# Performance work log

Hardware: AMD Instinct MI355X
Metric: run time of the kernel (lower is better)

## Reference

```python
import jax, jax.numpy as jnp
import numpy as np

ENC_DIM, PRED_DIM, JOINT_DIM, VOCAB = 512, 640, 512, 1024

def setup_inputs() -> dict:
    key = jax.random.key(0)
    ks = jax.random.split(key, 8)
    s = lambda d: 1.0 / np.sqrt(d)
    return {
        "enc_out": jax.random.normal(ks[0], (8, 256, ENC_DIM), jnp.float32),
        "pred_out": jax.random.normal(ks[1], (8, 64, PRED_DIM), jnp.float32),
        "W_enc": jax.random.uniform(ks[2], (ENC_DIM, JOINT_DIM), jnp.float32, -s(ENC_DIM), s(ENC_DIM)),
        "b_enc": jax.random.uniform(ks[3], (JOINT_DIM,), jnp.float32, -s(ENC_DIM), s(ENC_DIM)),
        "W_pred": jax.random.uniform(ks[4], (PRED_DIM, JOINT_DIM), jnp.float32, -s(PRED_DIM), s(PRED_DIM)),
        "b_pred": jax.random.uniform(ks[5], (JOINT_DIM,), jnp.float32, -s(PRED_DIM), s(PRED_DIM)),
        "W_joint": jax.random.uniform(ks[6], (JOINT_DIM, VOCAB), jnp.float32, -s(JOINT_DIM), s(JOINT_DIM)),
        "b_joint": jax.random.uniform(ks[7], (VOCAB,), jnp.float32, -s(JOINT_DIM), s(JOINT_DIM)),
    }

def reference(enc_out, pred_out, W_enc, b_enc, W_pred, b_pred, W_joint, b_joint):
    # (B,T,J) and (B,U,J) projections
    enc_p = jnp.einsum('btd,dj->btj', enc_out, W_enc) + b_enc
    pred_p = jnp.einsum('bud,dj->buj', pred_out, W_pred) + b_pred
    # broadcast add -> (B,T,U,J), tanh, project to vocab
    joint = jnp.tanh(enc_p[:, :, None, :] + pred_p[:, None, :, :])
    logits = jnp.einsum('btuj,jv->btuv', joint, W_joint) + b_joint
    return logits
```

## Files before the change

### kernel.cpp

```cpp
#include <hip/hip_runtime.h>
#include <hip/hip_bf16.h>
#include <stdint.h>

#define B_    8
#define T_    256
#define U_    64
#define JD    512
#define VD    1024
#define ROWS  (B_*T_*U_)
#define MTOT  (B_*T_)
#define UROWS (B_*U_)

typedef __attribute__((ext_vector_type(8))) short short8;
typedef __attribute__((ext_vector_type(4))) float f32x4;

__device__ __forceinline__ unsigned short f2bf(float f) {
  unsigned u = __float_as_uint(f);
  u += 0x7fffu + ((u >> 16) & 1u);
  return (unsigned short)(u >> 16);
}
__device__ __forceinline__ float fast_tanh(float x) {
  float e = __builtin_amdgcn_exp2f(x * 2.8853900817779268f);
  return 1.0f - 2.0f * __builtin_amdgcn_rcpf(e + 1.0f);
}

__device__ __forceinline__ void pack_w_body(const float* __restrict__ W,
                                            unsigned short* __restrict__ dst,
                                            int K, int N, int t) {
  int lane = t & 63;
  int rest = t >> 6;
  int kch  = K >> 5;
  int kc   = rest % kch;
  int nt   = rest / kch;
  int krow = (kc << 5) + ((lane >> 4) << 3);
  int col  = (nt << 4) + (lane & 15);
  unsigned short v[8];
#pragma unroll
  for (int j = 0; j < 8; ++j) v[j] = f2bf(W[(size_t)(krow + j) * N + col]);
  uint4 o;
  o.x = v[0] | ((unsigned)v[1] << 16);
  o.y = v[2] | ((unsigned)v[3] << 16);
  o.z = v[4] | ((unsigned)v[5] << 16);
  o.w = v[6] | ((unsigned)v[7] << 16);
  *(uint4*)(dst + ((size_t)t << 3)) = o;
}

__global__ void __launch_bounds__(256) k_pack_all(
    const float* __restrict__ We, const float* __restrict__ Wp,
    const float* __restrict__ Wj,
    unsigned short* __restrict__ de, unsigned short* __restrict__ dp,
    unsigned short* __restrict__ dj) {
  int blk = blockIdx.x;
  int tid = threadIdx.x;
  if (blk < 128)      pack_w_body(We, de, 512, 512,  blk * 256 + tid);
  else if (blk < 288) pack_w_body(Wp, dp, 640, 512,  (blk - 128) * 256 + tid);
  else                pack_w_body(Wj, dj, 512, 1024, (blk - 288) * 256 + tid);
}

__device__ __forceinline__ void proj_body(const float* __restrict__ A,
    const unsigned short* __restrict__ Bp, const float* __restrict__ bias,
    float* __restrict__ C, int M, int K, int N, int w, int lane) {
  int nw = N >> 6;
  int wm = w / nw, wn = w % nw;
  int m0 = wm << 4, n0 = wn << 6;
  if (m0 >= M) return;
  int kch = K >> 5;
  int q = lane >> 4, c = lane & 15;
  f32x4 acc[4] = {f32x4{0,0,0,0}, f32x4{0,0,0,0}, f32x4{0,0,0,0}, f32x4{0,0,0,0}};
  const float* arow = A + (size_t)(m0 + c) * K + (q << 3);
  for (int kc = 0; kc < kch; ++kc) {
    float4 a0 = *(const float4*)(arow + (kc << 5));
    float4 a1 = *(const float4*)(arow + (kc << 5) + 4);
    short8 a;
    a[0] = (short)f2bf(a0.x); a[1] = (short)f2bf(a0.y);
    a[2] = (short)f2bf(a0.z); a[3] = (short)f2bf(a0.w);
    a[4] = (short)f2bf(a1.x); a[5] = (short)f2bf(a1.y);
    a[6] = (short)f2bf(a1.z); a[7] = (short)f2bf(a1.w);
#pragma unroll
    for (int j = 0; j < 4; ++j) {
      size_t nt16 = (size_t)((n0 >> 4) + j);
      short8 b = *(const short8*)(Bp + (((nt16 * kch + kc) << 6) + lane) * 8);
      acc[j] = __builtin_amdgcn_mfma_f32_16x16x32_bf16(a, b, acc[j], 0, 0, 0);
    }
  }
#pragma unroll
  for (int j = 0; j < 4; ++j) {
    int col = n0 + (j << 4) + c;
    float bv = bias[col];
#pragma unroll
    for (int r = 0; r < 4; ++r) {
      int row = m0 + (q << 2) + r;
      C[(size_t)row * N + col] = acc[j][r] + bv;
    }
  }
}

__global__ void __launch_bounds__(256) k_proj_both(
    const float* __restrict__ enc_out, const float* __restrict__ pred_out,
    const unsigned short* __restrict__ Wep, const unsigned short* __restrict__ Wpp,
    const float* __restrict__ b_enc, const float* __restrict__ b_pred,
    float* __restrict__ enc_p, float* __restrict__ pred_p) {
  int blk  = blockIdx.x;
  int lane = threadIdx.x & 63;
  int wloc = threadIdx.x >> 6;
  if (blk < 256)
    proj_body(enc_out,  Wep, b_enc,  enc_p,  MTOT,  512, JD, blk * 4 + wloc, lane);
  else
    proj_body(pred_out, Wpp, b_pred, pred_p, UROWS, 640, JD, (blk - 256) * 4 + wloc, lane);
}

__global__ void __launch_bounds__(512, 4) k_fused(
    const float* __restrict__ enc_p, const float* __restrict__ pred_p,
    const unsigned short* __restrict__ Bp, const float* __restrict__ bias,
    float* __restrict__ out) {
  __shared__ unsigned short Alds[32 * 64 * 8];
  const short8* a8 = (const short8*)Alds;
  const short8* b8 = (const short8*)Bp;

  int bid  = blockIdx.x;
  int nt   = bid & 3;
  int mt   = bid >> 2;
  int tid  = threadIdx.x;
  int lane = tid & 63;
  int w    = tid >> 6;
  int wm   = w >> 2, wn = w & 3;
  int rb0w = wm << 2;
  int nt0w = (nt << 4) + (wn << 2);
  int c15  = lane & 15, q8 = (lane >> 4) << 3;

  f32x4 acc[4][4];
#pragma unroll
  for (int i = 0; i < 4; ++i)
#pragma unroll
    for (int j = 0; j < 4; ++j) acc[i][j] = f32x4{0, 0, 0, 0};

  for (int ch = 0; ch < 4; ++ch) {
    int kbase = ch << 7;
#pragma unroll 2
    for (int ff = 0; ff < 4; ++ff) {
      int f   = w + (ff << 3);
      int rb  = f >> 2, kcl = f & 3;
      int r   = (mt << 7) + (rb << 4) + c15;
      int k0  = kbase + (kcl << 5) + q8;
      const float* ep = enc_p  + ((size_t)(r >> 6) << 9) + k0;
      const float* pp = pred_p + ((size_t)(((r >> 14) << 6) + (r & 63)) << 9) + k0;
      float4 e0 = *(const float4*)ep, e1 = *(const float4*)(ep + 4);
      float4 p0 = *(const float4*)pp, p1 = *(const float4*)(pp + 4);
      unsigned short v[8];
      v[0] = f2bf(fast_tanh(e0.x + p0.x));
      v[1] = f2bf(fast_tanh(e0.y + p0.y));
      v[2] = f2bf(fast_tanh(e0.z + p0.z));
      v[3] = f2bf(fast_tanh(e0.w + p0.w));
      v[4] = f2bf(fast_tanh(e1.x + p1.x));
      v[5] = f2bf(fast_tanh(e1.y + p1.y));
      v[6] = f2bf(fast_tanh(e1.z + p1.z));
      v[7] = f2bf(fast_tanh(e1.w + p1.w));
      uint4 o;
      o.x = v[0] | ((unsigned)v[1] << 16);
      o.y = v[2] | ((unsigned)v[3] << 16);
      o.z = v[4] | ((unsigned)v[5] << 16);
      o.w = v[6] | ((unsigned)v[7] << 16);
      *(uint4*)(Alds + ((((rb << 2) + kcl) << 6) + lane) * 8) = o;
    }
    __syncthreads();
#pragma unroll
    for (int kcl = 0; kcl < 4; ++kcl) {
      int kc = (ch << 2) + kcl;
      short8 a[4], b[4];
#pragma unroll
      for (int i = 0; i < 4; ++i)
        a[i] = a8[(((rb0w + i) << 2) + kcl) * 64 + lane];
#pragma unroll
      for (int j = 0; j < 4; ++j)
        b[j] = b8[(((size_t)(nt0w + j) << 4) + kc) * 64 + lane];
#pragma unroll
      for (int i = 0; i < 4; ++i)
#pragma unroll
        for (int j = 0; j < 4; ++j)
          acc[i][j] = __builtin_amdgcn_mfma_f32_16x16x32_bf16(a[i], b[j], acc[i][j], 0, 0, 0);
    }
    __syncthreads();
  }

  int q = lane >> 4;
#pragma unroll
  for (int j = 0; j < 4; ++j) {
    int col = ((nt0w + j) << 4) + c15;
    float bv = bias[col];
#pragma unroll
    for (int i = 0; i < 4; ++i) {
      int row = (mt << 7) + ((rb0w + i) << 4) + (q << 2);
      size_t o = ((size_t)row << 10) + col;
#pragma unroll
      for (int rr = 0; rr < 4; ++rr)
        out[o + ((size_t)rr << 10)] = acc[i][j][rr] + bv;
    }
  }
}

__global__ void __launch_bounds__(256) k_proj_naive(
    const float* __restrict__ A, const float* __restrict__ W,
    const float* __restrict__ bias, float* __restrict__ C,
    int M, int K, int N) {
  int t = blockIdx.x * blockDim.x + threadIdx.x;
  if (t >= M * N) return;
  int row = t / N, col = t % N;
  float s = bias[col];
  for (int k = 0; k < K; ++k)
    s += A[(size_t)row * K + k] * W[(size_t)k * N + col];
  C[t] = s;
}
__global__ void __launch_bounds__(256) k_joint_naive(
    const float* __restrict__ enc_p, const float* __restrict__ pred_p,
    const float* __restrict__ Wj, const float* __restrict__ bj,
    float* __restrict__ out) {
  __shared__ float jrow[JD];
  int gr = blockIdx.x;
  int bt = gr >> 6;
  int bu = ((gr >> 14) << 6) + (gr & 63);
  for (int k = threadIdx.x; k < JD; k += 256)
    jrow[k] = fast_tanh(enc_p[(size_t)bt * JD + k] + pred_p[(size_t)bu * JD + k]);
  __syncthreads();
  int v0 = threadIdx.x * 4;
  float s0 = bj[v0], s1 = bj[v0 + 1], s2 = bj[v0 + 2], s3 = bj[v0 + 3];
  for (int k = 0; k < JD; ++k) {
    float jv = jrow[k];
    const float* wr = Wj + (size_t)k * VD + v0;
    s0 += jv * wr[0];
    s1 += jv * wr[1];
    s2 += jv * wr[2];
    s3 += jv * wr[3];
  }
  size_t o = ((size_t)gr << 10) + v0;
  out[o] = s0; out[o + 1] = s1; out[o + 2] = s2; out[o + 3] = s3;
}

extern "C" void kernel_launch(void* const* d_in, const int* in_sizes, int n_in,
                              void* d_out, int out_size, void* d_ws, size_t ws_size,
                              hipStream_t stream) {
  const float* enc_out  = (const float*)d_in[0];
  const float* pred_out = (const float*)d_in[1];
  const float* W_enc    = (const float*)d_in[2];
  const float* b_enc    = (const float*)d_in[3];
  const float* W_pred   = (const float*)d_in[4];
  const float* b_pred   = (const float*)d_in[5];
  const float* W_joint  = (const float*)d_in[6];
  const float* b_joint  = (const float*)d_in[7];
  float* out = (float*)d_out;

  char* ws = (char*)d_ws;
  size_t off = 0;
  auto alloc = [&](size_t bytes) -> char* {
    char* p = ws + off;
    off += (bytes + 255) & ~(size_t)255;
    return p;
  };
  float* enc_p  = (float*)alloc((size_t)MTOT * JD * 4);
  float* pred_p = (float*)alloc((size_t)UROWS * JD * 4);
  size_t small_need = off;
  unsigned short* Wenc_p  = (unsigned short*)alloc((size_t)512 * 512 * 2);
  unsigned short* Wpred_p = (unsigned short*)alloc((size_t)640 * 512 * 2);
  unsigned short* Wjnt_p  = (unsigned short*)alloc((size_t)512 * 1024 * 2);
  size_t big_need = off;

  if (ws_size >= big_need) {
    k_pack_all<<<544, 256, 0, stream>>>(W_enc, W_pred, W_joint,
                                        Wenc_p, Wpred_p, Wjnt_p);
    k_proj_both<<<320, 256, 0, stream>>>(enc_out, pred_out, Wenc_p, Wpred_p,
                                         b_enc, b_pred, enc_p, pred_p);
    k_fused<<<(ROWS / 128) * (VD / 256), 512, 0, stream>>>(enc_p, pred_p,
                                                           Wjnt_p, b_joint, out);
  } else if (ws_size >= small_need) {
    k_proj_naive<<<(MTOT * JD + 255) / 256, 256, 0, stream>>>(enc_out, W_enc, b_enc, enc_p, MTOT, 512, JD);
    k_proj_naive<<<(UROWS * JD + 255) / 256, 256, 0, stream>>>(pred_out, W_pred, b_pred, pred_p, UROWS, 640, JD);
    k_joint_naive<<<ROWS, 256, 0, stream>>>(enc_p, pred_p, W_joint, b_joint, out);
  }
  (void)in_sizes; (void)n_in; (void)out_size;
}
```

Before: 853.2 us.

## Double-buffer fused tanh A-tile in LDS and overlap its production with MFMA

Restructures the fused joint kernel so each K-chunk of the tanh(enc+pred) A tile goes into one of two small LDS buffers. The next chunk's global loads and tanh/bf16 packing now run alongside the current chunk's MFMAs, with one barrier per chunk instead of a bulk fill of four chunks followed by compute. It also remaps block IDs so neighbouring blocks spread across the grid, raises wave priority around the MFMA block, and writes output with nontemporal stores in row-major order. The aim is to hide activation load and transcendental latency behind matrix math and to cut LDS use, at the cost of more barriers and more live registers.

```diff
diff --git a/kernel.cpp b/kernel.cpp
--- a/kernel.cpp
+++ b/kernel.cpp
@@ -22,6 +22,24 @@
 __device__ __forceinline__ float fast_tanh(float x) {
   float e = __builtin_amdgcn_exp2f(x * 2.8853900817779268f);
   return 1.0f - 2.0f * __builtin_amdgcn_rcpf(e + 1.0f);
+}
+__device__ __forceinline__ uint4 tanh_pack8(float4 e0, float4 e1,
+                                            float4 p0, float4 p1) {
+  unsigned short v[8];
+  v[0] = f2bf(fast_tanh(e0.x + p0.x));
+  v[1] = f2bf(fast_tanh(e0.y + p0.y));
+  v[2] = f2bf(fast_tanh(e0.z + p0.z));
+  v[3] = f2bf(fast_tanh(e0.w + p0.w));
+  v[4] = f2bf(fast_tanh(e1.x + p1.x));
+  v[5] = f2bf(fast_tanh(e1.y + p1.y));
+  v[6] = f2bf(fast_tanh(e1.z + p1.z));
+  v[7] = f2bf(fast_tanh(e1.w + p1.w));
+  uint4 o;
+  o.x = v[0] | ((unsigned)v[1] << 16);
+  o.y = v[2] | ((unsigned)v[3] << 16);
+  o.z = v[4] | ((unsigned)v[5] << 16);
+  o.w = v[6] | ((unsigned)v[7] << 16);
+  return o;
 }
 
 __device__ __forceinline__ void pack_w_body(const float* __restrict__ W,
@@ -113,13 +131,12 @@
     const float* __restrict__ enc_p, const float* __restrict__ pred_p,
     const unsigned short* __restrict__ Bp, const float* __restrict__ bias,
     float* __restrict__ out) {
-  __shared__ unsigned short Alds[32 * 64 * 8];
-  const short8* a8 = (const short8*)Alds;
-  const short8* b8 = (const short8*)Bp;
+  __shared__ unsigned short Alds[2 * 8 * 64 * 8];
 
   int bid  = blockIdx.x;
-  int nt   = bid & 3;
-  int mt   = bid >> 2;
+  int swz  = ((bid & 7) << 9) + (bid >> 3);
+  int nt   = swz & 3;
+  int mt   = swz >> 2;
   int tid  = threadIdx.x;
   int lane = tid & 63;
   int w    = tid >> 6;
@@ -128,72 +145,71 @@
   int nt0w = (nt << 4) + (wn << 2);
   int c15  = lane & 15, q8 = (lane >> 4) << 3;
 
+  int r = (mt << 7) + (w << 4) + c15;
+  const float* ep = enc_p  + ((size_t)(r >> 6) << 9) + q8;
+  const float* pp = pred_p + ((size_t)(((r >> 14) << 6) + (r & 63)) << 9) + q8;
+  unsigned short* myA = Alds + (((w << 6) + lane) << 3);
+
+  const short8* b8 = (const short8*)Bp;
+
   f32x4 acc[4][4];
 #pragma unroll
   for (int i = 0; i < 4; ++i)
 #pragma unroll
     for (int j = 0; j < 4; ++j) acc[i][j] = f32x4{0, 0, 0, 0};
 
-  for (int ch = 0; ch < 4; ++ch) {
-    int kbase = ch << 7;
-#pragma unroll 2
-    for (int ff = 0; ff < 4; ++ff) {
-      int f   = w + (ff << 3);
-      int rb  = f >> 2, kcl = f & 3;
-      int r   = (mt << 7) + (rb << 4) + c15;
-      int k0  = kbase + (kcl << 5) + q8;
-      const float* ep = enc_p  + ((size_t)(r >> 6) << 9) + k0;
-      const float* pp = pred_p + ((size_t)(((r >> 14) << 6) + (r & 63)) << 9) + k0;
-      float4 e0 = *(const float4*)ep, e1 = *(const float4*)(ep + 4);
-      float4 p0 = *(const float4*)pp, p1 = *(const float4*)(pp + 4);
-      unsigned short v[8];
-      v[0] = f2bf(fast_tanh(e0.x + p0.x));
-      v[1] = f2bf(fast_tanh(e0.y + p0.y));
-      v[2] = f2bf(fast_tanh(e0.z + p0.z));
-      v[3] = f2bf(fast_tanh(e0.w + p0.w));
-      v[4] = f2bf(fast_tanh(e1.x + p1.x));
-      v[5] = f2bf(fast_tanh(e1.y + p1.y));
-      v[6] = f2bf(fast_tanh(e1.z + p1.z));
-      v[7] = f2bf(fast_tanh(e1.w + p1.w));
-      uint4 o;
-      o.x = v[0] | ((unsigned)v[1] << 16);
-      o.y = v[2] | ((unsigned)v[3] << 16);
-      o.z = v[4] | ((unsigned)v[5] << 16);
-      o.w = v[6] | ((unsigned)v[7] << 16);
-      *(uint4*)(Alds + ((((rb << 2) + kcl) << 6) + lane) * 8) = o;
-    }
+  {
+    float4 e0 = *(const float4*)ep,       e1 = *(const float4*)(ep + 4);
+    float4 p0 = *(const float4*)pp,       p1 = *(const float4*)(pp + 4);
+    *(uint4*)myA = tanh_pack8(e0, e1, p0, p1);
+  }
+  __syncthreads();
+
+  for (int kc = 0; kc < 16; ++kc) {
+    int cur = kc & 1;
+    float4 ne0, ne1, np0, np1;
+    if (kc < 15) {
+      const float* e = ep + ((kc + 1) << 5);
+      const float* p = pp + ((kc + 1) << 5);
+      ne0 = *(const float4*)e; ne1 = *(const float4*)(e + 4);
+      np0 = *(const float4*)p; np1 = *(const float4*)(p + 4);
+    }
+    short8 b[4];
+#pragma unroll
+    for (int j = 0; j < 4; ++j)
+      b[j] = b8[(((size_t)(nt0w + j) << 4) + kc) * 64 + lane];
+    const short8* abuf = (const short8*)(Alds + (cur << 12));
+    short8 a[4];
+#pragma unroll
+    for (int i = 0; i < 4; ++i)
+      a[i] = abuf[((rb0w + i) << 6) + lane];
+    __builtin_amdgcn_s_setprio(1);
+#pragma unroll
+    for (int i = 0; i < 4; ++i)
+#pragma unroll
+      for (int j = 0; j < 4; ++j)
+        acc[i][j] = __builtin_amdgcn_mfma_f32_16x16x32_bf16(a[i], b[j], acc[i][j], 0, 0, 0);
+    __builtin_amdgcn_s_setprio(0);
+    if (kc < 15)
+      *(uint4*)(myA + ((cur ^ 1) << 12)) = tanh_pack8(ne0, ne1, np0, np1);
     __syncthreads();
-#pragma unroll
-    for (int kcl = 0; kcl < 4; ++kcl) {
-      int kc = (ch << 2) + kcl;
-      short8 a[4], b[4];
-#pragma unroll
-      for (int i = 0; i < 4; ++i)
-        a[i] = a8[(((rb0w + i) << 2) + kcl) * 64 + lane];
-#pragma unroll
-      for (int j = 0; j < 4; ++j)
-        b[j] = b8[(((size_t)(nt0w + j) << 4) + kc) * 64 + lane];
-#pragma unroll
-      for (int i = 0; i < 4; ++i)
-#pragma unroll
-        for (int j = 0; j < 4; ++j)
-          acc[i][j] = __builtin_amdgcn_mfma_f32_16x16x32_bf16(a[i], b[j], acc[i][j], 0, 0, 0);
-    }
-    __syncthreads();
-  }
-
+  }
+
+  float bv[4];
+#pragma unroll
+  for (int j = 0; j < 4; ++j) bv[j] = bias[((nt0w + j) << 4) + c15];
   int q = lane >> 4;
 #pragma unroll
-  for (int j = 0; j < 4; ++j) {
-    int col = ((nt0w + j) << 4) + c15;
-    float bv = bias[col];
-#pragma unroll
-    for (int i = 0; i < 4; ++i) {
-      int row = (mt << 7) + ((rb0w + i) << 4) + (q << 2);
-      size_t o = ((size_t)row << 10) + col;
-#pragma unroll
-      for (int rr = 0; rr < 4; ++rr)
-        out[o + ((size_t)rr << 10)] = acc[i][j][rr] + bv;
+  for (int i = 0; i < 4; ++i) {
+#pragma unroll
+    for (int rr = 0; rr < 4; ++rr) {
+      int row = (mt << 7) + ((rb0w + i) << 4) + (q << 2) + rr;
+      size_t o = ((size_t)row << 10);
+#pragma unroll
+      for (int j = 0; j < 4; ++j) {
+        int col = ((nt0w + j) << 4) + c15;
+        __builtin_nontemporal_store(acc[i][j][rr] + bv[j], &out[o + col]);
+      }
     }
   }
 }
```

After: 793.3 us. 7.0% less time.
